# Kernel tuning notes

Measured on AMD Instinct MI355X. Metric: run time of the kernel, lower is better.

The kernel has to match this reference:

```python
import jax, jax.numpy as jnp
import numpy as np

B, T_FRAMES, T_TOKENS = 2048, 8192, 1024
MAX_DUR = 16.0


def setup_inputs() -> dict:
    key = jax.random.key(0)
    k1, k2, k3, k4 = jax.random.split(key, 4)
    frame_scalar = jax.random.normal(k1, (B, T_FRAMES), dtype=jnp.float32)
    # float durations as the duration predictor would emit (hard mode rounds them)
    duration = jax.random.uniform(k2, (B, T_TOKENS), dtype=jnp.float32) * MAX_DUR
    frame_scalar_len = jax.random.randint(k3, (B,), 1, T_FRAMES + 1, dtype=jnp.int32)
    duration_len = jax.random.randint(k4, (B,), 1, T_TOKENS + 1, dtype=jnp.int32)
    return {
        "frame_scalar": frame_scalar,
        "duration": duration,
        "frame_scalar_len": frame_scalar_len,
        "duration_len": duration_len,
    }


def reference(frame_scalar, duration, frame_scalar_len, duration_len):
    """Hard-mode duration-based frame->token scalar averaging (FastSpeech2).

    Equivalent to FastSpeech2Decoder.proc_duration (hard, min_frame_num=0,
    max_frame_num=None, reduction_factor=1) followed by
    average_scalar_by_duration with len_regulation_type='hard', vectorized via
    prefix sums instead of nested Python loops.
    """
    Bb, Tt = duration.shape
    # proc_duration: round + clamp to [0, inf)
    dur = jnp.clip(jnp.round(duration), 0.0, None)  # [B, T_tok]
    # zero out tokens beyond duration_len (loop only runs j < duration_len[i])
    tok_valid = jnp.arange(Tt, dtype=jnp.int32)[None, :] < duration_len[:, None]
    dur = jnp.where(tok_valid, dur, 0.0)
    # cumulative end positions, clipped at frame_scalar_len exactly like the
    # running-cursor clipping d = min(d, L - cursor) in the torch loop
    flen = frame_scalar_len.astype(jnp.float32)[:, None]  # [B,1]
    ends_f = jnp.minimum(jnp.cumsum(dur, axis=1), flen)    # [B, T_tok]
    starts_f = jnp.concatenate([jnp.zeros((Bb, 1), dtype=ends_f.dtype), ends_f[:, :-1]], axis=1)
    d = ends_f - starts_f  # effective (clipped) segment lengths
    # segment sums via exclusive prefix sum of frame_scalar: [B, T_frames+1]
    cfs = jnp.concatenate(
        [jnp.zeros((Bb, 1), dtype=jnp.float32), jnp.cumsum(frame_scalar, axis=1)], axis=1
    )
    e_idx = ends_f.astype(jnp.int32)
    s_idx = starts_f.astype(jnp.int32)
    seg_sum = jnp.take_along_axis(cfs, e_idx, axis=1) - jnp.take_along_axis(cfs, s_idx, axis=1)
    token_scalar = jnp.where(d > 0, seg_sum / jnp.maximum(d, 1.0), 0.0)  # [B, T_tok]
    return token_scalar, duration_len
```

## Files before the change

kernel.cpp:

```cpp
#include <hip/hip_runtime.h>


namespace {
constexpr int TT = 1024;
constexpr int TF = 8192;
constexpr int NT = 512;
constexpr int NW = NT / 64;

__device__ __forceinline__ float wave_scan_incl(float x) {
    float f = x;
    {
        int t_ = __builtin_amdgcn_update_dpp(0, __float_as_int(f), 0x111, 0xf, 0xf, false);
        f += __int_as_float(t_);
    }
    {
        int t_ = __builtin_amdgcn_update_dpp(0, __float_as_int(f), 0x112, 0xf, 0xf, false);
        f += __int_as_float(t_);
    }
    {
        int t_ = __builtin_amdgcn_update_dpp(0, __float_as_int(f), 0x114, 0xf, 0xf, false);
        f += __int_as_float(t_);
    }
    {
        int t_ = __builtin_amdgcn_update_dpp(0, __float_as_int(f), 0x118, 0xf, 0xf, false);
        f += __int_as_float(t_);
    }
    {
        int t_ = __builtin_amdgcn_update_dpp(0, __float_as_int(f), 0x142, 0xa, 0xf, false);
        f += __int_as_float(t_);
    }
    {
        int t_ = __builtin_amdgcn_update_dpp(0, __float_as_int(f), 0x143, 0xc, 0xf, false);
        f += __int_as_float(t_);
    }
    return f;
}
}

__global__ __launch_bounds__(NT, 8) void fs2_avg_kernel(
    const float* __restrict__ frame_scalar,
    const float* __restrict__ duration,
    const int* __restrict__ frame_scalar_len,
    const int* __restrict__ duration_len,
    float* __restrict__ out,
    int n_rows)
{
    __shared__ alignas(16) float s_wA[NW];

    const int b = blockIdx.x;
    const int t = threadIdx.x;
    const int lane = t & 63;
    const int wid = t >> 6;

    const int dlen = duration_len[b];
    const float flen = (float)frame_scalar_len[b];

    const float* frow = frame_scalar + (size_t)b * TF;

    const int j0 = t * 2;
    float2 d2 = (j0 < dlen)
        ? *reinterpret_cast<const float2*>(duration + (size_t)b * TT + j0)
        : make_float2(0.f, 0.f);
    float d0 = fmaxf(rintf(d2.x), 0.0f); if (j0 + 0 >= dlen) d0 = 0.0f;
    float d1 = fmaxf(rintf(d2.y), 0.0f); if (j0 + 1 >= dlen) d1 = 0.0f;
    const float c0 = d0, c1 = c0 + d1;

    const float ws = wave_scan_incl(c1);
    if (lane == 63) s_wA[wid] = ws;

    __syncthreads();

    const float4 wA0 = *reinterpret_cast<const float4*>(&s_wA[0]);
    const float4 wA1 = *reinterpret_cast<const float4*>(&s_wA[4]);
    float base = ws - c1;
    base += (wid > 0) ? wA0.x : 0.f;
    base += (wid > 1) ? wA0.y : 0.f;
    base += (wid > 2) ? wA0.z : 0.f;
    base += (wid > 3) ? wA0.w : 0.f;
    base += (wid > 4) ? wA1.x : 0.f;
    base += (wid > 5) ? wA1.y : 0.f;
    base += (wid > 6) ? wA1.z : 0.f;

    const float sprev0 = (j0 == 0) ? 0.0f : fminf(base, flen);
    const float e0 = fminf(base + c0, flen);
    const float e1 = fminf(base + c1, flen);

    const int si = (int)sprev0;
    const int mi = (int)e0;
    const int ei = (int)e1;

    float acc0 = 0.0f, acc1 = 0.0f;
    if (ei > si) {
        const int q0 = si >> 2;
        #pragma unroll
        for (int j = 0; j < 9; ++j) {
            const int q  = q0 + j;
            const int qc = (q < TF / 4 - 1) ? q : TF / 4 - 1;
            const float4 v = *reinterpret_cast<const float4*>(frow + 4 * qc);
            const int p0 = 4 * q;
            {
                const int p = p0 + 0; const float x = v.x;
                acc0 += (p >= si && p < mi) ? x : 0.f;
                acc1 += (p >= mi && p < ei) ? x : 0.f;
            }
            {
                const int p = p0 + 1; const float x = v.y;
                acc0 += (p >= si && p < mi) ? x : 0.f;
                acc1 += (p >= mi && p < ei) ? x : 0.f;
            }
            {
                const int p = p0 + 2; const float x = v.z;
                acc0 += (p >= si && p < mi) ? x : 0.f;
                acc1 += (p >= mi && p < ei) ? x : 0.f;
            }
            {
                const int p = p0 + 3; const float x = v.w;
                acc0 += (p >= si && p < mi) ? x : 0.f;
                acc1 += (p >= mi && p < ei) ? x : 0.f;
            }
        }
    }

    const float o0 = (mi > si) ? acc0 / (e0 - sprev0) : 0.0f;
    const float o1 = (ei > mi) ? acc1 / (e1 - e0) : 0.0f;

    *reinterpret_cast<float2*>(out + (size_t)b * TT + j0) = make_float2(o0, o1);

    if (t == 0) out[(size_t)n_rows * TT + b] = (float)dlen;
}

extern "C" void kernel_launch(void* const* d_in, const int* in_sizes, int n_in,
                              void* d_out, int out_size, void* d_ws, size_t ws_size,
                              hipStream_t stream) {
    const float* frame_scalar     = (const float*)d_in[0];
    const float* duration         = (const float*)d_in[1];
    const int*   frame_scalar_len = (const int*)d_in[2];
    const int*   duration_len     = (const int*)d_in[3];
    float* out = (float*)d_out;
    const int B = in_sizes[2];
    fs2_avg_kernel<<<B, NT, 0, stream>>>(frame_scalar, duration, frame_scalar_len,
                                         duration_len, out, B);
}
```

Before: 14.15 us.

## Stage the needed frame row into LDS with direct global-to-LDS loads

Each block now copies only the frame quads it will use (bounded by the clipped total duration and frame length) into shared memory with global_load_lds. The per-thread window sums then read from LDS instead of issuing overlapping uncoalesced global float4 loads. The inner accumulation is recast as a running total minus the first segment, and the divides become hardware reciprocals. The cost is a 32KB LDS footprint per block, which limits occupancy, and a dependence on correct vmcnt waits before the barrier. The approximate reciprocal may also slightly change results.

```diff
diff --git a/kernel.cpp b/kernel.cpp
--- a/kernel.cpp
+++ b/kernel.cpp
@@ -6,6 +6,8 @@
 constexpr int TF = 8192;
 constexpr int NT = 512;
 constexpr int NW = NT / 64;
+constexpr int QROW = TF / 4;
+constexpr int QPAD = QROW + 8;
 
 __device__ __forceinline__ float wave_scan_incl(float x) {
     float f = x;
@@ -35,6 +37,13 @@
     }
     return f;
 }
+
+__device__ __forceinline__ void stage_quad(const float* gsrc, float* lds_wave_base) {
+    __builtin_amdgcn_global_load_lds(
+        (const __attribute__((address_space(1))) void*)gsrc,
+        (__attribute__((address_space(3))) void*)lds_wave_base,
+        16, 0, 0);
+}
 }
 
 __global__ __launch_bounds__(NT, 8) void fs2_avg_kernel(
@@ -45,6 +54,7 @@
     float* __restrict__ out,
     int n_rows)
 {
+    __shared__ alignas(16) float s_frame[QPAD * 4];
     __shared__ alignas(16) float s_wA[NW];
 
     const int b = blockIdx.x;
@@ -53,9 +63,18 @@
     const int wid = t >> 6;
 
     const int dlen = duration_len[b];
-    const float flen = (float)frame_scalar_len[b];
+    const int flen_i = frame_scalar_len[b];
+    const float flen = (float)flen_i;
 
     const float* frow = frame_scalar + (size_t)b * TF;
+
+    const int Qf = (flen_i + 3) >> 2;
+    const int chunk0 = (Qf < NT) ? Qf : NT;
+    if (t < chunk0) {
+        stage_quad(frow + 4 * t, &s_frame[4 * (wid * 64)]);
+    }
+
+    if (t == 0) out[(size_t)n_rows * TT + b] = (float)dlen;
 
     const int j0 = t * 2;
     float2 d2 = (j0 < dlen)
@@ -81,6 +100,20 @@
     base += (wid > 5) ? wA1.y : 0.f;
     base += (wid > 6) ? wA1.z : 0.f;
 
+    const float total = wA0.x + wA0.y + wA0.z + wA0.w + wA1.x + wA1.y + wA1.z + wA1.w;
+    const float Fneed = fminf(total, flen);
+    const int Qneed = ((int)Fneed + 3) >> 2;
+    if (Qneed > NT) {
+        #pragma unroll
+        for (int r = 1; r < 4; ++r) {
+            const int q = r * NT + t;
+            if (q < Qneed) {
+                stage_quad(frow + 4 * q, &s_frame[4 * (r * NT + wid * 64)]);
+            }
+        }
+        __syncthreads();
+    }
+
     const float sprev0 = (j0 == 0) ? 0.0f : fminf(base, flen);
     const float e0 = fminf(base + c0, flen);
     const float e1 = fminf(base + c1, flen);
@@ -89,44 +122,40 @@
     const int mi = (int)e0;
     const int ei = (int)e1;
 
-    float acc0 = 0.0f, acc1 = 0.0f;
+    float acc0 = 0.0f, accT = 0.0f;
     if (ei > si) {
         const int q0 = si >> 2;
+        {
+            const float4 v = *reinterpret_cast<const float4*>(&s_frame[4 * q0]);
+            const int p0 = 4 * q0;
+            #pragma unroll
+            for (int e = 0; e < 4; ++e) {
+                const float x = (&v.x)[e];
+                const int p = p0 + e;
+                const bool ge = (p >= si);
+                accT += (ge & (p < ei)) ? x : 0.f;
+                acc0 += (ge & (p < mi)) ? x : 0.f;
+            }
+        }
         #pragma unroll
-        for (int j = 0; j < 9; ++j) {
-            const int q  = q0 + j;
-            const int qc = (q < TF / 4 - 1) ? q : TF / 4 - 1;
-            const float4 v = *reinterpret_cast<const float4*>(frow + 4 * qc);
+        for (int j = 1; j < 9; ++j) {
+            const int q = q0 + j;
+            const float4 v = *reinterpret_cast<const float4*>(&s_frame[4 * q]);
             const int p0 = 4 * q;
-            {
-                const int p = p0 + 0; const float x = v.x;
-                acc0 += (p >= si && p < mi) ? x : 0.f;
-                acc1 += (p >= mi && p < ei) ? x : 0.f;
-            }
-            {
-                const int p = p0 + 1; const float x = v.y;
-                acc0 += (p >= si && p < mi) ? x : 0.f;
-                acc1 += (p >= mi && p < ei) ? x : 0.f;
-            }
-            {
-                const int p = p0 + 2; const float x = v.z;
-                acc0 += (p >= si && p < mi) ? x : 0.f;
-                acc1 += (p >= mi && p < ei) ? x : 0.f;
-            }
-            {
-                const int p = p0 + 3; const float x = v.w;
-                acc0 += (p >= si && p < mi) ? x : 0.f;
-                acc1 += (p >= mi && p < ei) ? x : 0.f;
+            #pragma unroll
+            for (int e = 0; e < 4; ++e) {
+                const float x = (&v.x)[e];
+                const int p = p0 + e;
+                accT += (p < ei) ? x : 0.f;
+                acc0 += (p < mi) ? x : 0.f;
             }
         }
     }
 
-    const float o0 = (mi > si) ? acc0 / (e0 - sprev0) : 0.0f;
-    const float o1 = (ei > mi) ? acc1 / (e1 - e0) : 0.0f;
+    const float o0 = (mi > si) ? acc0 * __builtin_amdgcn_rcpf(e0 - sprev0) : 0.0f;
+    const float o1 = (ei > mi) ? (accT - acc0) * __builtin_amdgcn_rcpf(e1 - e0) : 0.0f;
 
     *reinterpret_cast<float2*>(out + (size_t)b * TT + j0) = make_float2(o0, o1);
-
-    if (t == 0) out[(size_t)n_rows * TT + b] = (float)dlen;
 }
 
 extern "C" void kernel_launch(void* const* d_in, const int* in_sizes, int n_in,
```

Result: slower. 16.12 us (+13.9%).

## Compute per-row frame prefix sum in LDS and index segments by differences

Applied to the files above, without the earlier changes.

Each block now loads the whole frame row (up to flen), builds an inclusive prefix sum across threads with a wave scan and a cross-wave combine, and stores it in a 32KB swizzled LDS array. Each segment sum then takes two LDS lookups instead of a masked 36-element gather from global memory per thread, and the division becomes a hardware reciprocal. The cost is reading the full valid row rather than only the touched frames, an extra barrier, and 32KB of LDS per block, which limits occupancy. Prefix-sum differences may also lose float precision compared with direct summation.

```diff
diff --git a/kernel.cpp b/kernel.cpp
--- a/kernel.cpp
+++ b/kernel.cpp
@@ -35,6 +35,12 @@
     }
     return f;
 }
+
+__device__ __forceinline__ int swz(int i) {
+    const int qi = i >> 2;
+    const int q2 = qi ^ ((qi >> 3) & 7);
+    return (q2 << 2) | (i & 3);
+}
 }
 
 __global__ __launch_bounds__(NT, 8) void fs2_avg_kernel(
@@ -45,7 +51,9 @@
     float* __restrict__ out,
     int n_rows)
 {
+    __shared__ alignas(16) float s_S[TF];
     __shared__ alignas(16) float s_wA[NW];
+    __shared__ alignas(16) float s_wF[NW];
 
     const int b = blockIdx.x;
     const int t = threadIdx.x;
@@ -53,9 +61,26 @@
     const int wid = t >> 6;
 
     const int dlen = duration_len[b];
-    const float flen = (float)frame_scalar_len[b];
+    const int flen_i = frame_scalar_len[b];
+    const float flen = (float)flen_i;
 
     const float* frow = frame_scalar + (size_t)b * TF;
+
+    if (t == 0) out[(size_t)n_rows * TT + b] = (float)dlen;
+
+    const int fb_idx = t * 16;
+    float f[16];
+    #pragma unroll
+    for (int j = 0; j < 4; ++j) {
+        float4 v = make_float4(0.f, 0.f, 0.f, 0.f);
+        if (fb_idx + 4 * j < flen_i)
+            v = *reinterpret_cast<const float4*>(frow + fb_idx + 4 * j);
+        f[4 * j + 0] = v.x; f[4 * j + 1] = v.y;
+        f[4 * j + 2] = v.z; f[4 * j + 3] = v.w;
+    }
+    #pragma unroll
+    for (int k = 1; k < 16; ++k) f[k] += f[k - 1];
+    const float ftot = f[15];
 
     const int j0 = t * 2;
     float2 d2 = (j0 < dlen)
@@ -65,8 +90,9 @@
     float d1 = fmaxf(rintf(d2.y), 0.0f); if (j0 + 1 >= dlen) d1 = 0.0f;
     const float c0 = d0, c1 = c0 + d1;
 
-    const float ws = wave_scan_incl(c1);
-    if (lane == 63) s_wA[wid] = ws;
+    const float ws  = wave_scan_incl(c1);
+    const float fsc = wave_scan_incl(ftot);
+    if (lane == 63) { s_wA[wid] = ws; s_wF[wid] = fsc; }
 
     __syncthreads();
 
@@ -81,6 +107,27 @@
     base += (wid > 5) ? wA1.y : 0.f;
     base += (wid > 6) ? wA1.z : 0.f;
 
+    const float4 wF0 = *reinterpret_cast<const float4*>(&s_wF[0]);
+    const float4 wF1 = *reinterpret_cast<const float4*>(&s_wF[4]);
+    float fbase = fsc - ftot;
+    fbase += (wid > 0) ? wF0.x : 0.f;
+    fbase += (wid > 1) ? wF0.y : 0.f;
+    fbase += (wid > 2) ? wF0.z : 0.f;
+    fbase += (wid > 3) ? wF0.w : 0.f;
+    fbase += (wid > 4) ? wF1.x : 0.f;
+    fbase += (wid > 5) ? wF1.y : 0.f;
+    fbase += (wid > 6) ? wF1.z : 0.f;
+
+    #pragma unroll
+    for (int j = 0; j < 4; ++j) {
+        const int i0 = fb_idx + 4 * j;
+        const float4 v = make_float4(fbase + f[4 * j + 0], fbase + f[4 * j + 1],
+                                     fbase + f[4 * j + 2], fbase + f[4 * j + 3]);
+        *reinterpret_cast<float4*>(&s_S[swz(i0)]) = v;
+    }
+
+    __syncthreads();
+
     const float sprev0 = (j0 == 0) ? 0.0f : fminf(base, flen);
     const float e0 = fminf(base + c0, flen);
     const float e1 = fminf(base + c1, flen);
@@ -89,44 +136,16 @@
     const int mi = (int)e0;
     const int ei = (int)e1;
 
-    float acc0 = 0.0f, acc1 = 0.0f;
+    float o0 = 0.0f, o1 = 0.0f;
     if (ei > si) {
-        const int q0 = si >> 2;
-        #pragma unroll
-        for (int j = 0; j < 9; ++j) {
-            const int q  = q0 + j;
-            const int qc = (q < TF / 4 - 1) ? q : TF / 4 - 1;
-            const float4 v = *reinterpret_cast<const float4*>(frow + 4 * qc);
-            const int p0 = 4 * q;
-            {
-                const int p = p0 + 0; const float x = v.x;
-                acc0 += (p >= si && p < mi) ? x : 0.f;
-                acc1 += (p >= mi && p < ei) ? x : 0.f;
-            }
-            {
-                const int p = p0 + 1; const float x = v.y;
-                acc0 += (p >= si && p < mi) ? x : 0.f;
-                acc1 += (p >= mi && p < ei) ? x : 0.f;
-            }
-            {
-                const int p = p0 + 2; const float x = v.z;
-                acc0 += (p >= si && p < mi) ? x : 0.f;
-                acc1 += (p >= mi && p < ei) ? x : 0.f;
-            }
-            {
-                const int p = p0 + 3; const float x = v.w;
-                acc0 += (p >= si && p < mi) ? x : 0.f;
-                acc1 += (p >= mi && p < ei) ? x : 0.f;
-            }
-        }
+        const float Gs = (si == 0) ? 0.0f : s_S[swz(si - 1)];
+        const float Gm = (mi == 0) ? 0.0f : s_S[swz(mi - 1)];
+        const float Ge = s_S[swz(ei - 1)];
+        o0 = (mi > si) ? (Gm - Gs) * __builtin_amdgcn_rcpf(e0 - sprev0) : 0.0f;
+        o1 = (ei > mi) ? (Ge - Gm) * __builtin_amdgcn_rcpf(e1 - e0) : 0.0f;
     }
 
-    const float o0 = (mi > si) ? acc0 / (e0 - sprev0) : 0.0f;
-    const float o1 = (ei > mi) ? acc1 / (e1 - e0) : 0.0f;
-
     *reinterpret_cast<float2*>(out + (size_t)b * TT + j0) = make_float2(o0, o1);
-
-    if (t == 0) out[(size_t)n_rows * TT + b] = (float)dlen;
 }
 
 extern "C" void kernel_launch(void* const* d_in, const int* in_sizes, int n_in,
```

Result: slower. 14.93 us (+5.5%).
